# Kernel tuning notes

Measured on AMD Instinct MI355X. Metric: run time of the kernel, lower is better.

Reference implementation:

```python
import jax, jax.numpy as jnp
import numpy as np

MASK_THRESH = 0.9
USED_PENALTY = 1e8


def setup_inputs() -> dict:
    key = jax.random.key(0)
    k1, k2, k3, k4 = jax.random.split(key, 4)
    B, C, H, W = 16, 1, 128, 128
    P, L = 16, 6            # num_protos, num_objects
    T = P * L               # candidate templates per image
    x = jax.random.uniform(k1, (B, C, H, W), jnp.float32)
    templates = jax.random.uniform(k2, (B, T, C, H, W), jnp.float32)
    masks = jax.random.uniform(k3, (B, T, 1, H, W), jnp.float32)
    background = jax.random.uniform(k4, (C, H, W), jnp.float32)
    return {"x": x, "templates": templates, "masks": masks,
            "background": background, "num_objects": L}


def reference(x, templates, masks, background, num_objects):
    """Greedy template selection (use_empty=True) + scene composition.

    Faithful to DecompModel4._greedy_selection + compose_templates:
    at each of L steps, every candidate template is composed UNDER the
    already-selected objects (compose paints last index first), the MSE vs
    the image is computed, the argmin candidate is selected, and non-empty
    candidates are masked out for future steps. Final reconstruction paints
    selected objects over the background with object 0 on top.
    """
    B, T, C, H, W = templates.shape
    L = num_objects
    dt = templates.dtype

    # prepend the empty template (index 0), as in use_empty=True
    temps = jnp.concatenate([jnp.zeros((B, 1, C, H, W), dt), templates], axis=1)  # (B,T+1,C,H,W)
    msks = jnp.concatenate([jnp.zeros((B, 1, 1, H, W), dt), masks], axis=1)       # (B,T+1,1,H,W)
    Tp1 = T + 1
    bidx = jnp.arange(B)
    bg = background[None]                      # (1,C,H,W)

    # candidate-over-background image, constant across greedy steps
    cand_cov = msks > MASK_THRESH              # (B,T+1,1,H,W)
    cand_img = jnp.where(cand_cov, temps * msks, bg[:, None])  # (B,T+1,C,H,W)

    # running canvas of already-selected objects (earlier selections on top)
    used = jnp.zeros((B, Tp1), bool)
    top_val = jnp.zeros((B, C, H, W), dt)
    top_cov = jnp.zeros((B, 1, H, W), bool)

    for _ in range(L):
        # selected stack painted over each candidate-over-background
        cur = jnp.where(top_cov[:, None], top_val[:, None], cand_img)  # (B,T+1,C,H,W)
        err = jnp.mean((x[:, None] - cur) ** 2, axis=(2, 3, 4))        # (B,T+1)
        err = jnp.where(used, USED_PENALTY, err)
        cid = jnp.argmin(err, axis=1)                                  # (B,)
        # mark as used, except the empty template (id 0) stays reusable
        used = used | ((jnp.arange(Tp1)[None, :] == cid[:, None]) & (cid != 0)[:, None])
        sel_obj = temps[bidx, cid]     # (B,C,H,W)
        sel_msk = msks[bidx, cid]      # (B,1,H,W)
        new_cov = sel_msk > MASK_THRESH
        # new selection goes UNDER already-selected pixels
        top_val = jnp.where((~top_cov) & new_cov, sel_obj * sel_msk, top_val)
        top_cov = top_cov | new_cov

    reconstruction = jnp.where(top_cov, top_val, bg)   # (B,C,H,W)
    return reconstruction
```

## Files before the change

### kernel.cpp

```cpp
#include <hip/hip_runtime.h>

#define B    16
#define T    96
#define TP1  97
#define HW   16384
#define HW4  4096
#define LSEL 6
#define THRESH 0.9f
#define SEG  512
#define CAP  2048

#define WS_CONTRIB 0
#define WS_USED    8192
#define WS_COUNTS  16384
#define WS_COV     41984
#define WS_CIDX    304128
#define WS_CVAL    6595584
#define WS_NEEDED  (WS_CVAL + (size_t)B * T * CAP * 4)

__global__ __launch_bounds__(256) void compact_kernel(
    const float* __restrict__ x, const float* __restrict__ temps,
    const float* __restrict__ msks, const float* __restrict__ bg,
    unsigned short* __restrict__ cidx, float* __restrict__ cval,
    int* __restrict__ counts, float* __restrict__ contrib)
{
    int slot = blockIdx.x;
    int b = slot / T, t = slot - b * T;
    const float4* t4  = ((const float4*)temps) + (size_t)slot * HW4;
    const float4* m4  = ((const float4*)msks)  + (size_t)slot * HW4;
    const float4* x4  = ((const float4*)x)     + (size_t)b * HW4;
    const float4* bg4 = (const float4*)bg;
    int wv = threadIdx.x >> 6, lane = threadIdx.x & 63;
    unsigned long long below = lane ? (~0ULL >> (64 - lane)) : 0ULL;
    unsigned short* sidx = cidx + (size_t)slot * CAP + wv * SEG;
    float*          sval = cval + (size_t)slot * CAP + wv * SEG;

    int off = 0;
    float sum = 0.f;
    int ib = wv * 1024 + lane;

    #pragma unroll
    for (int it = 0; it < 16; it += 4) {
        float4 tv[4], mv[4], xv[4], bv[4];
        #pragma unroll
        for (int u = 0; u < 4; ++u) {
            int i = ib + (it + u) * 64;
            tv[u] = t4[i]; mv[u] = m4[i]; xv[u] = x4[i]; bv[u] = bg4[i];
        }
        #pragma unroll
        for (int u = 0; u < 4; ++u) {
            int pix = (ib + (it + u) * 64) * 4;
            bool p0 = mv[u].x > THRESH, p1 = mv[u].y > THRESH,
                 p2 = mv[u].z > THRESH, p3 = mv[u].w > THRESH;
            float a0 = xv[u].x - tv[u].x * mv[u].x, c0 = xv[u].x - bv[u].x;
            float a1 = xv[u].y - tv[u].y * mv[u].y, c1 = xv[u].y - bv[u].y;
            float a2 = xv[u].z - tv[u].z * mv[u].z, c2 = xv[u].z - bv[u].z;
            float a3 = xv[u].w - tv[u].w * mv[u].w, c3 = xv[u].w - bv[u].w;
            float v0 = a0*a0 - c0*c0, v1 = a1*a1 - c1*c1;
            float v2 = a2*a2 - c2*c2, v3 = a3*a3 - c3*c3;
            unsigned long long B0 = __ballot(p0), B1 = __ballot(p1);
            unsigned long long B2 = __ballot(p2), B3 = __ballot(p3);
            int n0 = __popcll(B0), n1 = __popcll(B1), n2 = __popcll(B2), n3 = __popcll(B3);
            if (p0) { int pos = off + __popcll(B0 & below);
                      if (pos < SEG) { sidx[pos] = (unsigned short)(pix+0); sval[pos] = v0; sum += v0; } }
            if (p1) { int pos = off + n0 + __popcll(B1 & below);
                      if (pos < SEG) { sidx[pos] = (unsigned short)(pix+1); sval[pos] = v1; sum += v1; } }
            if (p2) { int pos = off + n0 + n1 + __popcll(B2 & below);
                      if (pos < SEG) { sidx[pos] = (unsigned short)(pix+2); sval[pos] = v2; sum += v2; } }
            if (p3) { int pos = off + n0 + n1 + n2 + __popcll(B3 & below);
                      if (pos < SEG) { sidx[pos] = (unsigned short)(pix+3); sval[pos] = v3; sum += v3; } }
            off += n0 + n1 + n2 + n3;
        }
    }

    #pragma unroll
    for (int o = 32; o > 0; o >>= 1) sum += __shfl_down(sum, o, 64);
    __shared__ float s[4];
    if (lane == 0) s[wv] = sum;
    __syncthreads();
    if (threadIdx.x == 0) contrib[b * TP1 + t + 1] = s[0] + s[1] + s[2] + s[3];
    if (lane == 0) counts[slot * 4 + wv] = (off < SEG) ? off : SEG;
}

__global__ __launch_bounds__(256) void step_contrib_kernel(
    const unsigned short* __restrict__ cidx, const float* __restrict__ cval,
    const int* __restrict__ counts, const unsigned char* __restrict__ top_cov,
    float* __restrict__ contrib)
{
    int slot = blockIdx.x;
    int b = slot / T, t = slot - b * T;
    int wv = threadIdx.x >> 6, lane = threadIdx.x & 63;
    int n = counts[slot * 4 + wv];
    const unsigned short* sidx = cidx + (size_t)slot * CAP + wv * SEG;
    const float*          sval = cval + (size_t)slot * CAP + wv * SEG;
    const unsigned char*  cov  = top_cov + (size_t)b * HW;

    float sum = 0.f;
    for (int i = lane; i < n; i += 64) {
        unsigned short p = sidx[i];
        float v = sval[i];
        if (!cov[p]) sum += v;
    }
    #pragma unroll
    for (int o = 32; o > 0; o >>= 1) sum += __shfl_down(sum, o, 64);
    __shared__ float s[4];
    if (lane == 0) s[wv] = sum;
    __syncthreads();
    if (threadIdx.x == 0) contrib[b * TP1 + t + 1] = s[0] + s[1] + s[2] + s[3];
}

__global__ __launch_bounds__(256) void sel_upd_kernel(
    const float* __restrict__ contrib, const float* __restrict__ temps,
    const float* __restrict__ msks, const float* __restrict__ bg,
    unsigned long long* __restrict__ used, unsigned char* __restrict__ top_cov,
    float* __restrict__ out, int first, int last)
{
    int b = blockIdx.y, g = blockIdx.x;
    int tid = threadIdx.x;
    __shared__ float sv[128];
    __shared__ int   si[128];
    __shared__ int   sc;
    if (tid < 128) {
        float v = 3.0e38f;
        if (tid < TP1) {
            if (tid == 0) v = 0.0f;
            else {
                v = contrib[b * TP1 + tid];
                if (!first && ((used[b * 2 + (tid >> 6)] >> (tid & 63)) & 1ULL)) v = 1.0e8f;
            }
        }
        sv[tid] = v; si[tid] = tid;
    }
    __syncthreads();
    for (int o = 64; o > 0; o >>= 1) {
        if (tid < o) {
            float v2 = sv[tid + o]; int i2 = si[tid + o];
            if (v2 < sv[tid] || (v2 == sv[tid] && i2 < si[tid])) { sv[tid] = v2; si[tid] = i2; }
        }
        __syncthreads();
    }
    if (tid == 0) sc = si[0];
    __syncthreads();
    int c = sc;

    if (!last && g == 0 && tid == 0) {
        if (first) {
            used[b * 2 + 0] = (c != 0 && c < 64) ? (1ULL << c) : 0ULL;
            used[b * 2 + 1] = (c >= 64) ? (1ULL << (c - 64)) : 0ULL;
        } else if (c != 0) {
            atomicOr(&used[b * 2 + (c >> 6)], 1ULL << (c & 63));
        }
    }

    uchar4* covp = (uchar4*)(top_cov + (size_t)b * HW);
    float4* valp = (float4*)(out + (size_t)b * HW);
    const float4* bg4 = (const float4*)bg;
    int k0 = g * 1024;

    if (!last) {
        if (c != 0) {
            size_t tb = (size_t)(b * T + c - 1) * HW4;
            const float4* t4 = ((const float4*)temps) + tb;
            const float4* m4 = ((const float4*)msks) + tb;
            for (int k = k0 + tid; k < k0 + 1024; k += 256) {
                float4 mv = m4[k], tv = t4[k];
                uchar4 cv; float4 vv;
                if (first) {
                    cv.x = mv.x > THRESH; cv.y = mv.y > THRESH;
                    cv.z = mv.z > THRESH; cv.w = mv.w > THRESH;
                    vv.x = tv.x * mv.x; vv.y = tv.y * mv.y;
                    vv.z = tv.z * mv.z; vv.w = tv.w * mv.w;
                } else {
                    cv = covp[k]; vv = valp[k];
                    if (mv.x > THRESH && !cv.x) { vv.x = tv.x * mv.x; cv.x = 1; }
                    if (mv.y > THRESH && !cv.y) { vv.y = tv.y * mv.y; cv.y = 1; }
                    if (mv.z > THRESH && !cv.z) { vv.z = tv.z * mv.z; cv.z = 1; }
                    if (mv.w > THRESH && !cv.w) { vv.w = tv.w * mv.w; cv.w = 1; }
                }
                covp[k] = cv; valp[k] = vv;
            }
        } else if (first) {
            for (int k = k0 + tid; k < k0 + 1024; k += 256)
                covp[k] = make_uchar4(0, 0, 0, 0);
        }
    } else {
        if (c != 0) {
            size_t tb = (size_t)(b * T + c - 1) * HW4;
            const float4* t4 = ((const float4*)temps) + tb;
            const float4* m4 = ((const float4*)msks) + tb;
            for (int k = k0 + tid; k < k0 + 1024; k += 256) {
                float4 mv = m4[k], tv = t4[k];
                uchar4 cv = covp[k];
                float4 vv = valp[k];
                float4 bv = bg4[k];
                vv.x = cv.x ? vv.x : (mv.x > THRESH ? tv.x * mv.x : bv.x);
                vv.y = cv.y ? vv.y : (mv.y > THRESH ? tv.y * mv.y : bv.y);
                vv.z = cv.z ? vv.z : (mv.z > THRESH ? tv.z * mv.z : bv.z);
                vv.w = cv.w ? vv.w : (mv.w > THRESH ? tv.w * mv.w : bv.w);
                valp[k] = vv;
            }
        } else {
            for (int k = k0 + tid; k < k0 + 1024; k += 256) {
                uchar4 cv = covp[k];
                float4 vv = valp[k];
                float4 bv = bg4[k];
                if (!cv.x) vv.x = bv.x;
                if (!cv.y) vv.y = bv.y;
                if (!cv.z) vv.z = bv.z;
                if (!cv.w) vv.w = bv.w;
                valp[k] = vv;
            }
        }
    }
}

__global__ __launch_bounds__(256) void contrib_full_kernel(
    const float* __restrict__ x, const float* __restrict__ temps,
    const float* __restrict__ msks, const float* __restrict__ bg,
    const unsigned char* __restrict__ top_cov, float* __restrict__ contrib,
    int first)
{
    int b = blockIdx.x / T;
    int t = blockIdx.x % T;
    size_t base = (size_t)(b * T + t) * HW;
    const float4* t4  = (const float4*)(temps + base);
    const float4* m4  = (const float4*)(msks + base);
    const float4* x4  = (const float4*)(x + (size_t)b * HW);
    const float4* bg4 = (const float4*)bg;
    const uchar4* c4  = (const uchar4*)(top_cov + (size_t)b * HW);
    float sum = 0.f;
    #pragma unroll 4
    for (int i = threadIdx.x; i < HW4; i += 256) {
        float4 tv = t4[i], mv = m4[i], xv = x4[i], bv = bg4[i];
        uchar4 cv = first ? make_uchar4(0,0,0,0) : c4[i];
        if (mv.x > THRESH && !cv.x) { float d1 = xv.x - tv.x*mv.x, d2 = xv.x - bv.x; sum += d1*d1 - d2*d2; }
        if (mv.y > THRESH && !cv.y) { float d1 = xv.y - tv.y*mv.y, d2 = xv.y - bv.y; sum += d1*d1 - d2*d2; }
        if (mv.z > THRESH && !cv.z) { float d1 = xv.z - tv.z*mv.z, d2 = xv.z - bv.z; sum += d1*d1 - d2*d2; }
        if (mv.w > THRESH && !cv.w) { float d1 = xv.w - tv.w*mv.w, d2 = xv.w - bv.w; sum += d1*d1 - d2*d2; }
    }
    #pragma unroll
    for (int o = 32; o > 0; o >>= 1) sum += __shfl_down(sum, o, 64);
    __shared__ float s[4];
    int lane = threadIdx.x & 63, wid = threadIdx.x >> 6;
    if (lane == 0) s[wid] = sum;
    __syncthreads();
    if (threadIdx.x == 0)
        contrib[b * TP1 + t + 1] = s[0] + s[1] + s[2] + s[3];
}

extern "C" void kernel_launch(void* const* d_in, const int* in_sizes, int n_in,
                              void* d_out, int out_size, void* d_ws, size_t ws_size,
                              hipStream_t stream) {
    const float* x     = (const float*)d_in[0];
    const float* temps = (const float*)d_in[1];
    const float* msks  = (const float*)d_in[2];
    const float* bg    = (const float*)d_in[3];

    char* ws = (char*)d_ws;
    float*              contrib = (float*)(ws + WS_CONTRIB);
    unsigned long long* used    = (unsigned long long*)(ws + WS_USED);
    int*                counts  = (int*)(ws + WS_COUNTS);
    unsigned char*      top_cov = (unsigned char*)(ws + WS_COV);
    unsigned short*     cidx    = (unsigned short*)(ws + WS_CIDX);
    float*              cval    = (float*)(ws + WS_CVAL);
    float*              out     = (float*)d_out;

    if (ws_size >= WS_NEEDED) {
        compact_kernel<<<B * T, 256, 0, stream>>>(x, temps, msks, bg,
                                                  cidx, cval, counts, contrib);
        sel_upd_kernel<<<dim3(4, B), 256, 0, stream>>>(contrib, temps, msks, bg,
                                                       used, top_cov, out, 1, 0);
        for (int l = 1; l < LSEL - 1; ++l) {
            step_contrib_kernel<<<B * T, 256, 0, stream>>>(cidx, cval, counts, top_cov, contrib);
            sel_upd_kernel<<<dim3(4, B), 256, 0, stream>>>(contrib, temps, msks, bg,
                                                           used, top_cov, out, 0, 0);
        }
        step_contrib_kernel<<<B * T, 256, 0, stream>>>(cidx, cval, counts, top_cov, contrib);
        sel_upd_kernel<<<dim3(4, B), 256, 0, stream>>>(contrib, temps, msks, bg,
                                                       used, top_cov, out, 0, 1);
    } else {
        contrib_full_kernel<<<B * T, 256, 0, stream>>>(x, temps, msks, bg, top_cov, contrib, 1);
        sel_upd_kernel<<<dim3(4, B), 256, 0, stream>>>(contrib, temps, msks, bg,
                                                       used, top_cov, out, 1, 0);
        for (int l = 1; l < LSEL - 1; ++l) {
            contrib_full_kernel<<<B * T, 256, 0, stream>>>(x, temps, msks, bg, top_cov, contrib, 0);
            sel_upd_kernel<<<dim3(4, B), 256, 0, stream>>>(contrib, temps, msks, bg,
                                                           used, top_cov, out, 0, 0);
        }
        contrib_full_kernel<<<B * T, 256, 0, stream>>>(x, temps, msks, bg, top_cov, contrib, 0);
        sel_upd_kernel<<<dim3(4, B), 256, 0, stream>>>(contrib, temps, msks, bg,
                                                       used, top_cov, out, 0, 1);
    }
}
```

Before: 301.6 us.

## Fuse argmin selection into step kernels via packed atomicMin and bitmask coverage

Replaces the separate per-step selection/update kernels with atomicMin on packed (error,cid) keys written by each candidate block, and lets every block of the next step rebuild the winner's coverage into a shared-memory bitmask from the compacted index lists. The final composition moves to one compose kernel that paints the six winners over the background. Compaction is staged in LDS and copied out coalesced. This halves the kernel-launch count and removes the byte coverage map, at the cost of redundant coverage rebuilds in every block and atomics on a few cells.

```diff
diff --git a/kernel.cpp b/kernel.cpp
--- a/kernel.cpp
+++ b/kernel.cpp
@@ -8,21 +8,32 @@
 #define LSEL 6
 #define THRESH 0.9f
 #define SEG  512
+#define SEGP (SEG + 64)
 #define CAP  2048
 
-#define WS_CONTRIB 0
-#define WS_USED    8192
-#define WS_COUNTS  16384
-#define WS_COV     41984
-#define WS_CIDX    304128
-#define WS_CVAL    6595584
+#define WS_CELLS   0
+#define WS_USED    1024
+#define WS_COVB    2048
+#define WS_COUNTS  36864
+#define WS_CIDX    65536
+#define WS_CVAL    (WS_CIDX + (size_t)B * T * CAP * 2)
 #define WS_NEEDED  (WS_CVAL + (size_t)B * T * CAP * 4)
+#define WS_CONTRF  0
+#define WS_COV8    65536
+
+#define EMPTY_KEY 0x8000000000000000ull
+
+__device__ __forceinline__ unsigned long long packkey(float v, int cid) {
+    unsigned int bits = __float_as_uint(v);
+    unsigned int ord = (bits & 0x80000000u) ? ~bits : (bits | 0x80000000u);
+    return ((unsigned long long)ord << 32) | (unsigned int)cid;
+}
 
 __global__ __launch_bounds__(256) void compact_kernel(
     const float* __restrict__ x, const float* __restrict__ temps,
     const float* __restrict__ msks, const float* __restrict__ bg,
     unsigned short* __restrict__ cidx, float* __restrict__ cval,
-    int* __restrict__ counts, float* __restrict__ contrib)
+    int* __restrict__ counts, unsigned long long* __restrict__ cells)
 {
     int slot = blockIdx.x;
     int b = slot / T, t = slot - b * T;
@@ -32,8 +43,10 @@
     const float4* bg4 = (const float4*)bg;
     int wv = threadIdx.x >> 6, lane = threadIdx.x & 63;
     unsigned long long below = lane ? (~0ULL >> (64 - lane)) : 0ULL;
-    unsigned short* sidx = cidx + (size_t)slot * CAP + wv * SEG;
-    float*          sval = cval + (size_t)slot * CAP + wv * SEG;
+
+    __shared__ unsigned short sidx[4][SEGP];
+    __shared__ float          sval[4][SEGP];
+    __shared__ float          ssum[4];
 
     int off = 0;
     float sum = 0.f;
@@ -61,52 +74,172 @@
             unsigned long long B0 = __ballot(p0), B1 = __ballot(p1);
             unsigned long long B2 = __ballot(p2), B3 = __ballot(p3);
             int n0 = __popcll(B0), n1 = __popcll(B1), n2 = __popcll(B2), n3 = __popcll(B3);
-            if (p0) { int pos = off + __popcll(B0 & below);
-                      if (pos < SEG) { sidx[pos] = (unsigned short)(pix+0); sval[pos] = v0; sum += v0; } }
-            if (p1) { int pos = off + n0 + __popcll(B1 & below);
-                      if (pos < SEG) { sidx[pos] = (unsigned short)(pix+1); sval[pos] = v1; sum += v1; } }
-            if (p2) { int pos = off + n0 + n1 + __popcll(B2 & below);
-                      if (pos < SEG) { sidx[pos] = (unsigned short)(pix+2); sval[pos] = v2; sum += v2; } }
-            if (p3) { int pos = off + n0 + n1 + n2 + __popcll(B3 & below);
-                      if (pos < SEG) { sidx[pos] = (unsigned short)(pix+3); sval[pos] = v3; sum += v3; } }
+
+            int pos0 = off + __popcll(B0 & below);
+            int pos1 = off + n0 + __popcll(B1 & below);
+            int pos2 = off + n0 + n1 + __popcll(B2 & below);
+            int pos3 = off + n0 + n1 + n2 + __popcll(B3 & below);
+            bool s0 = p0 && (pos0 < SEG), s1 = p1 && (pos1 < SEG);
+            bool s2 = p2 && (pos2 < SEG), s3 = p3 && (pos3 < SEG);
+            int a0i = s0 ? pos0 : SEG + lane;
+            int a1i = s1 ? pos1 : SEG + lane;
+            int a2i = s2 ? pos2 : SEG + lane;
+            int a3i = s3 ? pos3 : SEG + lane;
+            sidx[wv][a0i] = (unsigned short)(pix + 0); sval[wv][a0i] = v0;
+            sidx[wv][a1i] = (unsigned short)(pix + 1); sval[wv][a1i] = v1;
+            sidx[wv][a2i] = (unsigned short)(pix + 2); sval[wv][a2i] = v2;
+            sidx[wv][a3i] = (unsigned short)(pix + 3); sval[wv][a3i] = v3;
+            sum += s0 ? v0 : 0.f;
+            sum += s1 ? v1 : 0.f;
+            sum += s2 ? v2 : 0.f;
+            sum += s3 ? v3 : 0.f;
             off += n0 + n1 + n2 + n3;
         }
     }
 
+    #pragma unroll
+    for (int o = 32; o > 0; o >>= 1) sum += __shfl_down(sum, o, 64);
+
+    int n = off < SEG ? off : SEG;
+    unsigned short* gidx = cidx + (size_t)slot * CAP + wv * SEG;
+    float*          gval = cval + (size_t)slot * CAP + wv * SEG;
+    for (int i = lane; i < n; i += 64) {
+        gidx[i] = sidx[wv][i];
+        gval[i] = sval[wv][i];
+    }
+    if (lane == 0) { counts[slot * 4 + wv] = n; ssum[wv] = sum; }
+    __syncthreads();
+    if (threadIdx.x == 0) {
+        float total = ssum[0] + ssum[1] + ssum[2] + ssum[3];
+        atomicMin(&cells[b * LSEL + 0], packkey(total, t + 1));
+        if (t == 0) atomicMin(&cells[b * LSEL + 0], EMPTY_KEY);
+    }
+}
+
+__global__ __launch_bounds__(256) void step_kernel(
+    const unsigned short* __restrict__ cidx, const float* __restrict__ cval,
+    const int* __restrict__ counts, unsigned long long* __restrict__ covb,
+    unsigned long long* __restrict__ used, unsigned long long* __restrict__ cells,
+    int l)
+{
+    int slot = blockIdx.x;
+    int b = slot / T, t = slot - b * T;
+    int tid = threadIdx.x, wv = tid >> 6, lane = tid & 63;
+    __shared__ unsigned long long scov[256];
+    __shared__ float ssum[4];
+
+    unsigned long long wkey = cells[b * LSEL + (l - 1)];
+    int wcid = (int)(unsigned int)(wkey & 0xFFFFFFFFull);
+
+    scov[tid] = covb[b * 256 + tid];
+    __syncthreads();
+    if (wcid != 0) {
+        int ws = b * T + (wcid - 1);
+        int wn = counts[ws * 4 + wv];
+        const unsigned short* widx = cidx + (size_t)ws * CAP + wv * SEG;
+        for (int i = lane; i < wn; i += 64) {
+            int p = widx[i];
+            atomicOr(&scov[p >> 6], 1ULL << (p & 63));
+        }
+    }
+    __syncthreads();
+    if (t == 0) {
+        covb[b * 256 + tid] = scov[tid];
+        if (tid == 0 && wcid != 0)
+            atomicOr(&used[b * 2 + (wcid >> 6)], 1ULL << (wcid & 63));
+    }
+
+    int mycid = t + 1;
+    bool is_used = ((used[b * 2 + (mycid >> 6)] >> (mycid & 63)) & 1ULL) || (mycid == wcid);
+
+    float sum = 0.f;
+    if (!is_used) {
+        int n = counts[slot * 4 + wv];
+        const unsigned short* si = cidx + (size_t)slot * CAP + wv * SEG;
+        const float*          sv = cval + (size_t)slot * CAP + wv * SEG;
+        for (int i = lane; i < n; i += 64) {
+            int p = si[i];
+            float v = sv[i];
+            if (!((scov[p >> 6] >> (p & 63)) & 1ULL)) sum += v;
+        }
+    }
+    #pragma unroll
+    for (int o = 32; o > 0; o >>= 1) sum += __shfl_down(sum, o, 64);
+    if (lane == 0) ssum[wv] = sum;
+    __syncthreads();
+    if (tid == 0) {
+        if (!is_used) {
+            float total = ssum[0] + ssum[1] + ssum[2] + ssum[3];
+            atomicMin(&cells[b * LSEL + l], packkey(total, mycid));
+        }
+        if (t == 0) atomicMin(&cells[b * LSEL + l], EMPTY_KEY);
+    }
+}
+
+__global__ __launch_bounds__(256) void compose_kernel(
+    const float* __restrict__ temps, const float* __restrict__ msks,
+    const float* __restrict__ bg, const unsigned long long* __restrict__ cells,
+    float* __restrict__ out)
+{
+    int b = blockIdx.y, g = blockIdx.x;
+    int tid = threadIdx.x;
+    int w[LSEL];
+    #pragma unroll
+    for (int l = 0; l < LSEL; ++l)
+        w[l] = (int)(unsigned int)(cells[b * LSEL + l] & 0xFFFFFFFFull);
+    const float4* bg4 = (const float4*)bg;
+    float4* o4 = ((float4*)out) + (size_t)b * HW4;
+    int k0 = g * 512;
+    for (int k = k0 + tid; k < k0 + 512; k += 256) {
+        float4 o = bg4[k];
+        #pragma unroll
+        for (int l = LSEL - 1; l >= 0; --l) {
+            if (w[l] != 0) {
+                size_t tb = ((size_t)(b * T + w[l] - 1)) * HW4 + k;
+                float4 mv = ((const float4*)msks)[tb];
+                float4 tv = ((const float4*)temps)[tb];
+                if (mv.x > THRESH) o.x = tv.x * mv.x;
+                if (mv.y > THRESH) o.y = tv.y * mv.y;
+                if (mv.z > THRESH) o.z = tv.z * mv.z;
+                if (mv.w > THRESH) o.w = tv.w * mv.w;
+            }
+        }
+        o4[k] = o;
+    }
+}
+
+__global__ __launch_bounds__(256) void contrib_full_kernel(
+    const float* __restrict__ x, const float* __restrict__ temps,
+    const float* __restrict__ msks, const float* __restrict__ bg,
+    const unsigned char* __restrict__ top_cov, float* __restrict__ contrib,
+    int first)
+{
+    int b = blockIdx.x / T;
+    int t = blockIdx.x % T;
+    size_t base = (size_t)(b * T + t) * HW;
+    const float4* t4  = (const float4*)(temps + base);
+    const float4* m4  = (const float4*)(msks + base);
+    const float4* x4  = (const float4*)(x + (size_t)b * HW);
+    const float4* bg4 = (const float4*)bg;
+    const uchar4* c4  = (const uchar4*)(top_cov + (size_t)b * HW);
+    float sum = 0.f;
+    #pragma unroll 4
+    for (int i = threadIdx.x; i < HW4; i += 256) {
+        float4 tv = t4[i], mv = m4[i], xv = x4[i], bv = bg4[i];
+        uchar4 cv = first ? make_uchar4(0,0,0,0) : c4[i];
+        if (mv.x > THRESH && !cv.x) { float d1 = xv.x - tv.x*mv.x, d2 = xv.x - bv.x; sum += d1*d1 - d2*d2; }
+        if (mv.y > THRESH && !cv.y) { float d1 = xv.y - tv.y*mv.y, d2 = xv.y - bv.y; sum += d1*d1 - d2*d2; }
+        if (mv.z > THRESH && !cv.z) { float d1 = xv.z - tv.z*mv.z, d2 = xv.z - bv.z; sum += d1*d1 - d2*d2; }
+        if (mv.w > THRESH && !cv.w) { float d1 = xv.w - tv.w*mv.w, d2 = xv.w - bv.w; sum += d1*d1 - d2*d2; }
+    }
     #pragma unroll
     for (int o = 32; o > 0; o >>= 1) sum += __shfl_down(sum, o, 64);
     __shared__ float s[4];
-    if (lane == 0) s[wv] = sum;
-    __syncthreads();
-    if (threadIdx.x == 0) contrib[b * TP1 + t + 1] = s[0] + s[1] + s[2] + s[3];
-    if (lane == 0) counts[slot * 4 + wv] = (off < SEG) ? off : SEG;
-}
-
-__global__ __launch_bounds__(256) void step_contrib_kernel(
-    const unsigned short* __restrict__ cidx, const float* __restrict__ cval,
-    const int* __restrict__ counts, const unsigned char* __restrict__ top_cov,
-    float* __restrict__ contrib)
-{
-    int slot = blockIdx.x;
-    int b = slot / T, t = slot - b * T;
-    int wv = threadIdx.x >> 6, lane = threadIdx.x & 63;
-    int n = counts[slot * 4 + wv];
-    const unsigned short* sidx = cidx + (size_t)slot * CAP + wv * SEG;
-    const float*          sval = cval + (size_t)slot * CAP + wv * SEG;
-    const unsigned char*  cov  = top_cov + (size_t)b * HW;
-
-    float sum = 0.f;
-    for (int i = lane; i < n; i += 64) {
-        unsigned short p = sidx[i];
-        float v = sval[i];
-        if (!cov[p]) sum += v;
-    }
-    #pragma unroll
-    for (int o = 32; o > 0; o >>= 1) sum += __shfl_down(sum, o, 64);
-    __shared__ float s[4];
-    if (lane == 0) s[wv] = sum;
-    __syncthreads();
-    if (threadIdx.x == 0) contrib[b * TP1 + t + 1] = s[0] + s[1] + s[2] + s[3];
+    int lane = threadIdx.x & 63, wid = threadIdx.x >> 6;
+    if (lane == 0) s[wid] = sum;
+    __syncthreads();
+    if (threadIdx.x == 0)
+        contrib[b * TP1 + t + 1] = s[0] + s[1] + s[2] + s[3];
 }
 
 __global__ __launch_bounds__(256) void sel_upd_kernel(
@@ -214,40 +347,6 @@
     }
 }
 
-__global__ __launch_bounds__(256) void contrib_full_kernel(
-    const float* __restrict__ x, const float* __restrict__ temps,
-    const float* __restrict__ msks, const float* __restrict__ bg,
-    const unsigned char* __restrict__ top_cov, float* __restrict__ contrib,
-    int first)
-{
-    int b = blockIdx.x / T;
-    int t = blockIdx.x % T;
-    size_t base = (size_t)(b * T + t) * HW;
-    const float4* t4  = (const float4*)(temps + base);
-    const float4* m4  = (const float4*)(msks + base);
-    const float4* x4  = (const float4*)(x + (size_t)b * HW);
-    const float4* bg4 = (const float4*)bg;
-    const uchar4* c4  = (const uchar4*)(top_cov + (size_t)b * HW);
-    float sum = 0.f;
-    #pragma unroll 4
-    for (int i = threadIdx.x; i < HW4; i += 256) {
-        float4 tv = t4[i], mv = m4[i], xv = x4[i], bv = bg4[i];
-        uchar4 cv = first ? make_uchar4(0,0,0,0) : c4[i];
-        if (mv.x > THRESH && !cv.x) { float d1 = xv.x - tv.x*mv.x, d2 = xv.x - bv.x; sum += d1*d1 - d2*d2; }
-        if (mv.y > THRESH && !cv.y) { float d1 = xv.y - tv.y*mv.y, d2 = xv.y - bv.y; sum += d1*d1 - d2*d2; }
-        if (mv.z > THRESH && !cv.z) { float d1 = xv.z - tv.z*mv.z, d2 = xv.z - bv.z; sum += d1*d1 - d2*d2; }
-        if (mv.w > THRESH && !cv.w) { float d1 = xv.w - tv.w*mv.w, d2 = xv.w - bv.w; sum += d1*d1 - d2*d2; }
-    }
-    #pragma unroll
-    for (int o = 32; o > 0; o >>= 1) sum += __shfl_down(sum, o, 64);
-    __shared__ float s[4];
-    int lane = threadIdx.x & 63, wid = threadIdx.x >> 6;
-    if (lane == 0) s[wid] = sum;
-    __syncthreads();
-    if (threadIdx.x == 0)
-        contrib[b * TP1 + t + 1] = s[0] + s[1] + s[2] + s[3];
-}
-
 extern "C" void kernel_launch(void* const* d_in, const int* in_sizes, int n_in,
                               void* d_out, int out_size, void* d_ws, size_t ws_size,
                               hipStream_t stream) {
@@ -257,28 +356,30 @@
     const float* bg    = (const float*)d_in[3];
 
     char* ws = (char*)d_ws;
-    float*              contrib = (float*)(ws + WS_CONTRIB);
-    unsigned long long* used    = (unsigned long long*)(ws + WS_USED);
-    int*                counts  = (int*)(ws + WS_COUNTS);
-    unsigned char*      top_cov = (unsigned char*)(ws + WS_COV);
-    unsigned short*     cidx    = (unsigned short*)(ws + WS_CIDX);
-    float*              cval    = (float*)(ws + WS_CVAL);
-    float*              out     = (float*)d_out;
+    float* out = (float*)d_out;
 
     if (ws_size >= WS_NEEDED) {
+        unsigned long long* cells = (unsigned long long*)(ws + WS_CELLS);
+        unsigned long long* used  = (unsigned long long*)(ws + WS_USED);
+        unsigned long long* covb  = (unsigned long long*)(ws + WS_COVB);
+        int*                counts= (int*)(ws + WS_COUNTS);
+        unsigned short*     cidx  = (unsigned short*)(ws + WS_CIDX);
+        float*              cval  = (float*)(ws + WS_CVAL);
+
+        hipMemsetAsync(ws + WS_CELLS, 0xFF, B * LSEL * 8, stream);
+        hipMemsetAsync(ws + WS_USED, 0, (WS_COVB - WS_USED) + B * 256 * 8, stream);
+
         compact_kernel<<<B * T, 256, 0, stream>>>(x, temps, msks, bg,
-                                                  cidx, cval, counts, contrib);
-        sel_upd_kernel<<<dim3(4, B), 256, 0, stream>>>(contrib, temps, msks, bg,
-                                                       used, top_cov, out, 1, 0);
-        for (int l = 1; l < LSEL - 1; ++l) {
-            step_contrib_kernel<<<B * T, 256, 0, stream>>>(cidx, cval, counts, top_cov, contrib);
-            sel_upd_kernel<<<dim3(4, B), 256, 0, stream>>>(contrib, temps, msks, bg,
-                                                           used, top_cov, out, 0, 0);
-        }
-        step_contrib_kernel<<<B * T, 256, 0, stream>>>(cidx, cval, counts, top_cov, contrib);
-        sel_upd_kernel<<<dim3(4, B), 256, 0, stream>>>(contrib, temps, msks, bg,
-                                                       used, top_cov, out, 0, 1);
+                                                  cidx, cval, counts, cells);
+        for (int l = 1; l < LSEL; ++l)
+            step_kernel<<<B * T, 256, 0, stream>>>(cidx, cval, counts, covb,
+                                                   used, cells, l);
+        compose_kernel<<<dim3(8, B), 256, 0, stream>>>(temps, msks, bg, cells, out);
     } else {
+        float*              contrib = (float*)(ws + WS_CONTRF);
+        unsigned long long* used    = (unsigned long long*)(ws + WS_USED);
+        unsigned char*      top_cov = (unsigned char*)(ws + WS_COV8);
+
         contrib_full_kernel<<<B * T, 256, 0, stream>>>(x, temps, msks, bg, top_cov, contrib, 1);
         sel_upd_kernel<<<dim3(4, B), 256, 0, stream>>>(contrib, temps, msks, bg,
                                                        used, top_cov, out, 1, 0);
```

Result: faster. 294.8 us (-2.3%).
